# Kernel optimization log

Measured on AMD Instinct MI355X. Metric: run time of the kernel, lower is better.

Reference implementation:

```python
import jax, jax.numpy as jnp
import numpy as np

L, T, D = 3, 65536, 256


def setup_inputs() -> dict:
    key = jax.random.key(0)
    ks = jax.random.split(key, 10)
    stdv = 1.0 / np.sqrt(D)
    u = lambda k, shape: jax.random.uniform(k, shape, jnp.float32, -stdv, stdv)
    return {
        "story": jax.random.normal(ks[0], (T, D), jnp.float32),
        "question": jax.random.normal(ks[1], (D,), jnp.float32),
        "Wz_f": u(ks[2], (L, D, D)),
        "bz_f": u(ks[3], (L, D)),
        "Wh_f": u(ks[4], (L, 2 * D, D)),
        "bh_f": u(ks[5], (L, D)),
        "Wz_b": u(ks[6], (L, D, D)),
        "bz_b": u(ks[7], (L, D)),
        "Wh_b": u(ks[8], (L, 2 * D, D)),
        "bh_b": u(ks[9], (L, D)),
    }


def _qrn_dir(x, q, Wz, bz, Wh, bh):
    """One QRN layer in one direction. x, q: [T, D]. Returns h states [T, D]."""
    z = jax.nn.sigmoid((x * q) @ Wz + bz)                      # [T, D]
    h_tilde = jnp.tanh(jnp.concatenate([x, q], axis=-1) @ Wh + bh)  # [T, D]
    a = 1.0 - z            # multiplicative factor on h_prev
    b = z * h_tilde        # additive term
    # linear recurrence h_t = a_t * h_{t-1} + b_t, h_0 = 0 -> associative scan
    def comb(c1, c2):
        a1, b1 = c1
        a2, b2 = c2
        return a1 * a2, a2 * b1 + b2
    _, h = jax.lax.associative_scan(comb, (a, b), axis=0)
    return h  # h[t] = hidden state after statement t


def reference(story, question, Wz_f, bz_f, Wh_f, bh_f, Wz_b, bz_b, Wh_b, bh_b):
    q = jnp.broadcast_to(question, story.shape)  # layer-0 question per step
    for layer in range(L):
        h_fwd = _qrn_dir(story, q, Wz_f[layer], bz_f[layer], Wh_f[layer], bh_f[layer])
        # backward direction: reversed story with correspondingly reversed questions
        h_bwd_rev = _qrn_dir(story[::-1], q[::-1], Wz_b[layer], bz_b[layer],
                             Wh_b[layer], bh_b[layer])
        if layer < L - 1:
            # q_{t}^{k+1} = h_fwd_t + h_bwd_t (aligned back to forward order)
            q = h_fwd + h_bwd_rev[::-1]
    return h_fwd[-1]  # final forward hidden state of last layer, [D]
```

## Files before the change

### kernel.cpp

```cpp
#include <hip/hip_runtime.h>
#include <hip/hip_bf16.h>
#include <math.h>

#define D    256
#define BT   128
#define GN   128
#define NSEG 32

typedef unsigned short u16;
typedef unsigned int   u32;
typedef __attribute__((ext_vector_type(8))) short short8;
typedef __attribute__((ext_vector_type(4))) float floatx4;

__device__ __forceinline__ float b2f(u16 v) {
    union { unsigned u; float f; } x; x.u = ((unsigned)v) << 16; return x.f;
}
__device__ __forceinline__ u16 f2b(float f) {
    union { unsigned u; float f; } x; x.f = f;
    unsigned lsb = (x.u >> 16) & 1;
    x.u += 0x7fffu + lsb;
    return (u16)(x.u >> 16);
}
__device__ __forceinline__ float sigm(float x) {
    return __builtin_amdgcn_rcpf(1.0f + __expf(-x));
}
__device__ __forceinline__ float tanhfast(float x) {
    return 1.0f - 2.0f * __builtin_amdgcn_rcpf(__expf(2.0f * x) + 1.0f);
}
__device__ __forceinline__ void async16(const u16* g, u16* l) {
    __builtin_amdgcn_global_load_lds(
        (const __attribute__((address_space(1))) unsigned int*)g,
        (__attribute__((address_space(3))) unsigned int*)l, 16, 0, 0);
}

__global__ __launch_bounds__(256) void wtrans_kernel(
    const float* __restrict__ question,
    const float* __restrict__ Wz_f, const float* __restrict__ Wh_f,
    const float* __restrict__ Wz_b, const float* __restrict__ Wh_b,
    u16* __restrict__ wt)
{
    int id = blockIdx.x * 256 + threadIdx.x;
    int combo = id / (3 * 65536);
    int rem   = id % (3 * 65536);
    int m = rem >> 16;
    int e = rem & 65535;
    int k = e >> 8, n = e & 255;
    int l   = combo < 3 ? combo : combo - 3;
    int dir = combo < 3 ? 0 : 1;
    float v;
    if (m == 0) {
        const float* Wz = dir ? Wz_b : Wz_f;
        v = Wz[((size_t)l * D + k) * D + n];
        if (l == 0) v *= question[k];
    } else {
        const float* Wh = dir ? Wh_b : Wh_f;
        int kk = (m == 2) ? (k + D) : k;
        v = Wh[((size_t)l * 2 * D + kk) * D + n];
    }
    wt[(size_t)combo * 3 * 65536 + (size_t)m * 65536 + (size_t)n * D + k] = f2b(v);
}

__global__ __launch_bounds__(256) void bias0_kernel(
    const float* __restrict__ question,
    const float* __restrict__ Wh_f, const float* __restrict__ Wh_b,
    const float* __restrict__ bh_f, const float* __restrict__ bh_b,
    float* __restrict__ bh0f, float* __restrict__ bh0b)
{
    const float* Wh = blockIdx.x ? Wh_b : Wh_f;
    const float* bh = blockIdx.x ? bh_b : bh_f;
    float* out = blockIdx.x ? bh0b : bh0f;
    int n = threadIdx.x;
    float acc = bh[n];
    for (int k = 0; k < D; ++k)
        acc = fmaf(question[k], Wh[(size_t)(D + k) * D + n], acc);
    out[n] = acc;
}

__global__ __launch_bounds__(256) void prep0_kernel(
    const float* __restrict__ story, u16* __restrict__ xb)
{
    long id = (long)blockIdx.x * 256 + threadIdx.x;
    const float* xp = story + id * 8;
    float4 xa = *(const float4*)xp;
    float4 xc = *(const float4*)(xp + 4);
    float xv[8] = {xa.x, xa.y, xa.z, xa.w, xc.x, xc.y, xc.z, xc.w};
    short8 xs;
    #pragma unroll
    for (int i = 0; i < 8; ++i) xs[i] = (short)f2b(xv[i]);
    *(short8*)(xb + id * 8) = xs;
}

struct StageS {
    u16 ax [2][BT * 32]; u16 aq [2][BT * 32]; u16 axq[2][BT * 32];
    u16 bz_[GN * 32]; u16 bx_[GN * 32]; u16 bq_[GN * 32];
};
struct Stage0 {
    u16 ax [2][BT * 32];
    u16 bz_[GN * 32]; u16 bx_[GN * 32];
};
struct EpiP  { float segA[NSEG][GN]; float segB[NSEG][GN]; };
union __align__(16) SharedP  { StageS st; EpiP ep; };
union __align__(16) SharedP0 { Stage0 st; EpiP ep; };

__device__ __forceinline__ void gate_epilogue(
    EpiP& ep, int tid, int t0, int n0,
    floatx4 (&accz)[4][2], floatx4 (&acch)[4][2],
    const float* bz, const float* bh,
    float* aggA, float* aggB, u32* abg, int FWD)
{
    const int lane = tid & 63, w = tid >> 6;
    const int wr = w & 1, wc = w >> 1;
    const int lr = lane & 15, quad = lane >> 4;

    float bzn[2], bhn[2];
    #pragma unroll
    for (int ct = 0; ct < 2; ++ct) {
        int n = n0 + wc * 32 + ct * 16 + lr;
        bzn[ct] = bz[n]; bhn[ct] = bh[n];
    }
    float av[4][2][4], bvv[4][2][4];
    #pragma unroll
    for (int rt = 0; rt < 4; ++rt) {
        #pragma unroll
        for (int ct = 0; ct < 2; ++ct) {
            #pragma unroll
            for (int r = 0; r < 4; ++r) {
                float z  = sigm(accz[rt][ct][r] + bzn[ct]);
                float ht = tanhfast(acch[rt][ct][r] + bhn[ct]);
                av[rt][ct][r]  = 1.0f - z;
                bvv[rt][ct][r] = z * ht;
            }
            float A = 1.f, B = 0.f;
            if (FWD) {
                #pragma unroll
                for (int r = 0; r < 4; ++r) { A = av[rt][ct][r] * A; B = fmaf(av[rt][ct][r], B, bvv[rt][ct][r]); }
            } else {
                #pragma unroll
                for (int r = 3; r >= 0; --r) { A = av[rt][ct][r] * A; B = fmaf(av[rt][ct][r], B, bvv[rt][ct][r]); }
            }
            int seg = wr * 16 + rt * 4 + quad;
            int col = wc * 32 + ct * 16 + lr;
            ep.segA[seg][col] = A;
            ep.segB[seg][col] = B;
        }
    }
    __syncthreads();

    if (tid < GN) {
        float A = 1.f, B = 0.f;
        if (FWD) {
            #pragma unroll
            for (int sg = 0; sg < NSEG; ++sg) {
                float a = ep.segA[sg][tid], b = ep.segB[sg][tid];
                ep.segA[sg][tid] = A; ep.segB[sg][tid] = B;
                A = a * A; B = fmaf(a, B, b);
            }
        } else {
            #pragma unroll
            for (int sg = NSEG - 1; sg >= 0; --sg) {
                float a = ep.segA[sg][tid], b = ep.segB[sg][tid];
                ep.segA[sg][tid] = A; ep.segB[sg][tid] = B;
                A = a * A; B = fmaf(a, B, b);
            }
        }
        int c = t0 / BT;
        aggA[(size_t)c * D + n0 + tid] = A;
        aggB[(size_t)c * D + n0 + tid] = B;
    }

    if (abg) {
        __syncthreads();
        #pragma unroll
        for (int rt = 0; rt < 4; ++rt) {
            #pragma unroll
            for (int ct = 0; ct < 2; ++ct) {
                int seg = wr * 16 + rt * 4 + quad;
                int col = wc * 32 + ct * 16 + lr;
                float Pa = ep.segA[seg][col];
                float Pb = ep.segB[seg][col];
                size_t base = (size_t)(t0 + wr * 64 + rt * 16 + quad * 4) * D + n0 + col;
                if (FWD) {
                    #pragma unroll
                    for (int r = 0; r < 4; ++r) {
                        Pa = av[rt][ct][r] * Pa;
                        Pb = fmaf(av[rt][ct][r], Pb, bvv[rt][ct][r]);
                        abg[base + (size_t)r * D] = (u32)f2b(Pa) | ((u32)f2b(Pb) << 16);
                    }
                } else {
                    #pragma unroll
                    for (int r = 3; r >= 0; --r) {
                        Pa = av[rt][ct][r] * Pa;
                        Pb = fmaf(av[rt][ct][r], Pb, bvv[rt][ct][r]);
                        abg[base + (size_t)r * D] = (u32)f2b(Pa) | ((u32)f2b(Pb) << 16);
                    }
                }
            }
        }
    }
}

__device__ __forceinline__ void gemm_body(
    SharedP& sh, int tid, int c, int n0,
    const u16* xbg, const u16* qg, const u16* xqg, const u16* wt,
    const float* bz, const float* bh,
    float* aggA, float* aggB, u32* abg, int FWD)
{
    const int t0   = c * BT;
    const int lane = tid & 63, w = tid >> 6;
    const int wr = w & 1, wc = w >> 1;
    const int lr   = lane & 15, quad = lane >> 4;

    const int swA   = (quad ^ ((lr >> 1) & 3)) * 8;
    const int offA0 = (wr * 64 + lr) * 32 + swA;
    const int offB0 = (wc * 32 + lr) * 32 + swA;

    floatx4 accz[4][2], acch[4][2];
    #pragma unroll
    for (int rt = 0; rt < 4; ++rt)
        #pragma unroll
        for (int ct = 0; ct < 2; ++ct) {
            accz[rt][ct] = (floatx4){0.f,0.f,0.f,0.f};
            acch[rt][ct] = (floatx4){0.f,0.f,0.f,0.f};
        }

    const int lb = (tid & ~63) * 8;

    const int arow = tid >> 2;
    const int agg_ = (tid & 3) ^ ((arow >> 1) & 3);
    const size_t goA = (size_t)(t0 + arow) * D + agg_ * 8;
    const size_t goB = (size_t)(n0 + arow) * D + agg_ * 8;
    const u16* pax  = xbg + goA;
    const u16* paq  = qg  + goA;
    const u16* paxq = xqg + goA;
    const u16* pbz  = wt + goB;
    const u16* pbx  = wt + 65536  + goB;
    const u16* pbq  = wt + 131072 + goB;

    async16(pax , sh.st.ax [0] + lb);
    async16(paq , sh.st.aq [0] + lb);
    async16(paxq, sh.st.axq[0] + lb);

    #pragma unroll
    for (int kk = 0; kk < 8; ++kk) {
        const int cur = kk & 1, nxt = cur ^ 1;
        const int k0 = kk * 32;
        async16(pbz + k0, sh.st.bz_ + lb);
        async16(pbx + k0, sh.st.bx_ + lb);
        async16(pbq + k0, sh.st.bq_ + lb);
        if (kk < 7) {
            async16(pax  + k0 + 32, sh.st.ax [nxt] + lb);
            async16(paq  + k0 + 32, sh.st.aq [nxt] + lb);
            async16(paxq + k0 + 32, sh.st.axq[nxt] + lb);
            asm volatile("s_waitcnt vmcnt(3)" ::: "memory");
        } else {
            asm volatile("s_waitcnt vmcnt(0)" ::: "memory");
        }
        __builtin_amdgcn_s_barrier();
        asm volatile("" ::: "memory");

        short8 vz[2], vx[2], vq[2];
        #pragma unroll
        for (int ct = 0; ct < 2; ++ct) {
            vz[ct] = *(const short8*)(sh.st.bz_ + offB0 + ct * 512);
            vx[ct] = *(const short8*)(sh.st.bx_ + offB0 + ct * 512);
            vq[ct] = *(const short8*)(sh.st.bq_ + offB0 + ct * 512);
        }
        #pragma unroll
        for (int rt = 0; rt < 4; ++rt) {
            short8 fxq = *(const short8*)(sh.st.axq[cur] + offA0 + rt * 512);
            short8 fx  = *(const short8*)(sh.st.ax [cur] + offA0 + rt * 512);
            short8 fq  = *(const short8*)(sh.st.aq [cur] + offA0 + rt * 512);
            #pragma unroll
            for (int ct = 0; ct < 2; ++ct) {
                accz[rt][ct] = __builtin_amdgcn_mfma_f32_16x16x32_bf16(fxq, vz[ct], accz[rt][ct], 0, 0, 0);
                acch[rt][ct] = __builtin_amdgcn_mfma_f32_16x16x32_bf16(fx , vx[ct], acch[rt][ct], 0, 0, 0);
                acch[rt][ct] = __builtin_amdgcn_mfma_f32_16x16x32_bf16(fq , vq[ct], acch[rt][ct], 0, 0, 0);
            }
        }
        asm volatile("" ::: "memory");
        __builtin_amdgcn_s_barrier();
        asm volatile("" ::: "memory");
    }

    gate_epilogue(sh.ep, tid, t0, n0, accz, acch, bz, bh, aggA, aggB, abg, FWD);
}

__device__ __forceinline__ void gemm0_body(
    SharedP0& sh, int tid, int c, int n0,
    const u16* xbg, const u16* wt,
    const float* bz, const float* bh0,
    float* aggA, float* aggB, u32* abg, int FWD)
{
    const int t0   = c * BT;
    const int lane = tid & 63, w = tid >> 6;
    const int wr = w & 1, wc = w >> 1;
    const int lr   = lane & 15, quad = lane >> 4;

    const int swA   = (quad ^ ((lr >> 1) & 3)) * 8;
    const int offA0 = (wr * 64 + lr) * 32 + swA;
    const int offB0 = (wc * 32 + lr) * 32 + swA;

    floatx4 accz[4][2], acch[4][2];
    #pragma unroll
    for (int rt = 0; rt < 4; ++rt)
        #pragma unroll
        for (int ct = 0; ct < 2; ++ct) {
            accz[rt][ct] = (floatx4){0.f,0.f,0.f,0.f};
            acch[rt][ct] = (floatx4){0.f,0.f,0.f,0.f};
        }

    const int lb = (tid & ~63) * 8;
    const int arow = tid >> 2;
    const int agg_ = (tid & 3) ^ ((arow >> 1) & 3);
    const size_t goA = (size_t)(t0 + arow) * D + agg_ * 8;
    const size_t goB = (size_t)(n0 + arow) * D + agg_ * 8;
    const u16* pax = xbg + goA;
    const u16* pbz = wt + goB;
    const u16* pbx = wt + 65536 + goB;

    async16(pax, sh.st.ax[0] + lb);

    #pragma unroll
    for (int kk = 0; kk < 8; ++kk) {
        const int cur = kk & 1, nxt = cur ^ 1;
        const int k0 = kk * 32;
        async16(pbz + k0, sh.st.bz_ + lb);
        async16(pbx + k0, sh.st.bx_ + lb);
        if (kk < 7) {
            async16(pax + k0 + 32, sh.st.ax[nxt] + lb);
            asm volatile("s_waitcnt vmcnt(1)" ::: "memory");
        } else {
            asm volatile("s_waitcnt vmcnt(0)" ::: "memory");
        }
        __builtin_amdgcn_s_barrier();
        asm volatile("" ::: "memory");

        short8 vz[2], vx[2];
        #pragma unroll
        for (int ct = 0; ct < 2; ++ct) {
            vz[ct] = *(const short8*)(sh.st.bz_ + offB0 + ct * 512);
            vx[ct] = *(const short8*)(sh.st.bx_ + offB0 + ct * 512);
        }
        #pragma unroll
        for (int rt = 0; rt < 4; ++rt) {
            short8 fx = *(const short8*)(sh.st.ax[cur] + offA0 + rt * 512);
            #pragma unroll
            for (int ct = 0; ct < 2; ++ct) {
                accz[rt][ct] = __builtin_amdgcn_mfma_f32_16x16x32_bf16(fx, vz[ct], accz[rt][ct], 0, 0, 0);
                acch[rt][ct] = __builtin_amdgcn_mfma_f32_16x16x32_bf16(fx, vx[ct], acch[rt][ct], 0, 0, 0);
            }
        }
        asm volatile("" ::: "memory");
        __builtin_amdgcn_s_barrier();
        asm volatile("" ::: "memory");
    }

    gate_epilogue(sh.ep, tid, t0, n0, accz, acch, bz, bh0, aggA, aggB, abg, FWD);
}

template<int FWD, int ABOUT>
__global__ __launch_bounds__(512, 4) void qrn_g5(
    const u16* __restrict__ xbg, const u16* __restrict__ qg,
    const u16* __restrict__ xqg, const u16* __restrict__ wt,
    const float* __restrict__ bz, const float* __restrict__ bh,
    float* __restrict__ aggA, float* __restrict__ aggB,
    u32* __restrict__ abg)
{
    __shared__ SharedP sh;
    const int tid  = threadIdx.x;
    const int bid  = (int)blockIdx.x;
    const int gidx = (bid & 7) * 128 + (bid >> 3);
    gemm_body(sh, tid, gidx >> 1, (gidx & 1) * GN,
              xbg, qg, xqg, wt, bz, bh, aggA, aggB, ABOUT ? abg : nullptr, FWD);
}

__global__ __launch_bounds__(512, 4) void qrn_gboth(
    const u16* __restrict__ xbg, const u16* __restrict__ qg,
    const u16* __restrict__ xqg,
    const u16* __restrict__ wtF, const u16* __restrict__ wtB,
    const float* __restrict__ bzf, const float* __restrict__ bhf,
    const float* __restrict__ bzb, const float* __restrict__ bhb,
    float* __restrict__ aggAf, float* __restrict__ aggBf,
    float* __restrict__ aggAb, float* __restrict__ aggBb,
    u32* __restrict__ abf, u32* __restrict__ abb)
{
    __shared__ SharedP sh;
    const int tid  = threadIdx.x;
    const int half = (int)blockIdx.x >> 10;
    const int bid  = (int)blockIdx.x & 1023;
    const int gidx = (bid & 7) * 128 + (bid >> 3);
    gemm_body(sh, tid, gidx >> 1, (gidx & 1) * GN,
              xbg, qg, xqg,
              half ? wtB : wtF,
              half ? bzb : bzf, half ? bhb : bhf,
              half ? aggAb : aggAf, half ? aggBb : aggBf,
              half ? abb : abf, half ? 0 : 1);
}

template<int FWD>
__global__ __launch_bounds__(512, 4) void qrn_g0(
    const u16* __restrict__ xbg, const u16* __restrict__ wt,
    const float* __restrict__ bz, const float* __restrict__ bh0,
    float* __restrict__ aggA, float* __restrict__ aggB,
    u32* __restrict__ abg)
{
    __shared__ SharedP0 sh;
    const int tid  = threadIdx.x;
    const int bid  = (int)blockIdx.x;
    const int gidx = (bid & 7) * 128 + (bid >> 3);
    gemm0_body(sh, tid, gidx >> 1, (gidx & 1) * GN,
               xbg, wt, bz, bh0, aggA, aggB, abg, FWD);
}

__global__ __launch_bounds__(512, 4) void qrn_g0both(
    const u16* __restrict__ xbg,
    const u16* __restrict__ wtF, const u16* __restrict__ wtB,
    const float* __restrict__ bzf, const float* __restrict__ bh0f,
    const float* __restrict__ bzb, const float* __restrict__ bh0b,
    float* __restrict__ aggAf, float* __restrict__ aggBf,
    float* __restrict__ aggAb, float* __restrict__ aggBb,
    u32* __restrict__ abf, u32* __restrict__ abb)
{
    __shared__ SharedP0 sh;
    const int tid  = threadIdx.x;
    const int half = (int)blockIdx.x >> 10;
    const int bid  = (int)blockIdx.x & 1023;
    const int gidx = (bid & 7) * 128 + (bid >> 3);
    gemm0_body(sh, tid, gidx >> 1, (gidx & 1) * GN,
               xbg,
               half ? wtB : wtF,
               half ? bzb : bzf, half ? bh0b : bh0f,
               half ? aggAb : aggAf, half ? aggBb : aggBf,
               half ? abb : abf, half ? 0 : 1);
}

__global__ __launch_bounds__(256) void replay2_fb(
    const u32* __restrict__ abf, const u32* __restrict__ abb,
    const float* __restrict__ hinif, const float* __restrict__ hinib,
    const u16* __restrict__ xb, u16* __restrict__ qout, u16* __restrict__ xq,
    int total8)
{
    for (int id = (int)blockIdx.x * 256 + (int)threadIdx.x; id < total8;
         id += (int)gridDim.x * 256) {
        int t  = id >> 5;
        int n0 = (id & 31) * 8;
        int c  = t >> 7;
        size_t o  = (size_t)t * D + n0;
        size_t hc = (size_t)c * D + n0;
        uint4 f0 = *(const uint4*)(abf + o);
        uint4 f1 = *(const uint4*)(abf + o + 4);
        uint4 g0 = *(const uint4*)(abb + o);
        uint4 g1 = *(const uint4*)(abb + o + 4);
        float4 hf0 = *(const float4*)(hinif + hc);
        float4 hf1 = *(const float4*)(hinif + hc + 4);
        float4 hb0 = *(const float4*)(hinib + hc);
        float4 hb1 = *(const float4*)(hinib + hc + 4);
        short8 xv = *(const short8*)(xb + o);
        u32 fa[8] = {f0.x, f0.y, f0.z, f0.w, f1.x, f1.y, f1.z, f1.w};
        u32 ga[8] = {g0.x, g0.y, g0.z, g0.w, g1.x, g1.y, g1.z, g1.w};
        float hfv[8] = {hf0.x, hf0.y, hf0.z, hf0.w, hf1.x, hf1.y, hf1.z, hf1.w};
        float hbv[8] = {hb0.x, hb0.y, hb0.z, hb0.w, hb1.x, hb1.y, hb1.z, hb1.w};
        short8 qs, xqs;
        #pragma unroll
        for (int i = 0; i < 8; ++i) {
            float hF = fmaf(b2f((u16)(fa[i] & 0xffff)), hfv[i], b2f((u16)(fa[i] >> 16)));
            float hB = fmaf(b2f((u16)(ga[i] & 0xffff)), hbv[i], b2f((u16)(ga[i] >> 16)));
            u16 qb = f2b(hF + hB);
            qs[i]  = (short)qb;
            xqs[i] = (short)f2b(b2f((u16)xv[i]) * b2f(qb));
        }
        *(short8*)(qout + o) = qs;
        *(short8*)(xq + o)   = xqs;
    }
}

__global__ __launch_bounds__(256) void replay2_f(
    const u32* __restrict__ abg, const float* __restrict__ hini,
    u16* __restrict__ qout, int total8)
{
    for (int id = (int)blockIdx.x * 256 + (int)threadIdx.x; id < total8;
         id += (int)gridDim.x * 256) {
        int t  = id >> 5;
        int n0 = (id & 31) * 8;
        int c  = t >> 7;
        size_t o  = (size_t)t * D + n0;
        size_t hc = (size_t)c * D + n0;
        uint4 f0 = *(const uint4*)(abg + o);
        uint4 f1 = *(const uint4*)(abg + o + 4);
        float4 hf0 = *(const float4*)(hini + hc);
        float4 hf1 = *(const float4*)(hini + hc + 4);
        u32 fa[8] = {f0.x, f0.y, f0.z, f0.w, f1.x, f1.y, f1.z, f1.w};
        float hfv[8] = {hf0.x, hf0.y, hf0.z, hf0.w, hf1.x, hf1.y, hf1.z, hf1.w};
        short8 qs;
        #pragma unroll
        for (int i = 0; i < 8; ++i) {
            float hF = fmaf(b2f((u16)(fa[i] & 0xffff)), hfv[i], b2f((u16)(fa[i] >> 16)));
            qs[i] = (short)f2b(hF);
        }
        *(short8*)(qout + o) = qs;
    }
}

__global__ __launch_bounds__(256) void replay2_b(
    const u32* __restrict__ abg, const float* __restrict__ hini,
    const u16* __restrict__ xb, u16* __restrict__ qout, u16* __restrict__ xq,
    int total8)
{
    for (int id = (int)blockIdx.x * 256 + (int)threadIdx.x; id < total8;
         id += (int)gridDim.x * 256) {
        int t  = id >> 5;
        int n0 = (id & 31) * 8;
        int c  = t >> 7;
        size_t o  = (size_t)t * D + n0;
        size_t hc = (size_t)c * D + n0;
        uint4 g0 = *(const uint4*)(abg + o);
        uint4 g1 = *(const uint4*)(abg + o + 4);
        float4 hb0 = *(const float4*)(hini + hc);
        float4 hb1 = *(const float4*)(hini + hc + 4);
        short8 qold = *(const short8*)(qout + o);
        short8 xv   = *(const short8*)(xb + o);
        u32 ga[8] = {g0.x, g0.y, g0.z, g0.w, g1.x, g1.y, g1.z, g1.w};
        float hbv[8] = {hb0.x, hb0.y, hb0.z, hb0.w, hb1.x, hb1.y, hb1.z, hb1.w};
        short8 qs, xqs;
        #pragma unroll
        for (int i = 0; i < 8; ++i) {
            float hB = fmaf(b2f((u16)(ga[i] & 0xffff)), hbv[i], b2f((u16)(ga[i] >> 16)));
            float qn = b2f((u16)qold[i]) + hB;
            u16 qb = f2b(qn);
            qs[i]  = (short)qb;
            xqs[i] = (short)f2b(b2f((u16)xv[i]) * b2f(qb));
        }
        *(short8*)(qout + o) = qs;
        *(short8*)(xq + o)   = xqs;
    }
}

__device__ __forceinline__ void scan_body(
    const float* aggA, const float* aggB, float* hinit, float* out_final,
    int fwd, int nch, int n, int tid)
{
    __shared__ float sA[256], sB[256];
    const int per = nch >> 8;
    float lA[4], lB[4];
    float A = 1.f, B = 0.f;
    for (int j = 0; j < per; ++j) {
        int pidx = tid * per + j;
        int c = fwd ? pidx : (nch - 1 - pidx);
        float a = aggA[(size_t)c * D + n];
        float b = aggB[(size_t)c * D + n];
        lA[j] = a; lB[j] = b;
        A = a * A;
        B = fmaf(a, B, b);
    }
    sA[tid] = A; sB[tid] = B;
    __syncthreads();
    for (int off = 1; off < 256; off <<= 1) {
        float pA = 1.f, pB = 0.f;
        if (tid >= off) { pA = sA[tid - off]; pB = sB[tid - off]; }
        __syncthreads();
        if (tid >= off) {
            float cA = sA[tid], cB = sB[tid];
            sA[tid] = pA * cA;
            sB[tid] = fmaf(cA, pB, cB);
        }
        __syncthreads();
    }
    float eB = (tid > 0) ? sB[tid - 1] : 0.f;
    for (int j = 0; j < per; ++j) {
        int pidx = tid * per + j;
        int c = fwd ? pidx : (nch - 1 - pidx);
        hinit[(size_t)c * D + n] = eB;
        eB = fmaf(lA[j], eB, lB[j]);
    }
    if (out_final != nullptr && tid == 0) out_final[n] = sB[255];
}

__global__ __launch_bounds__(256) void scan_p2_kernel(
    const float* __restrict__ aggA, const float* __restrict__ aggB,
    float* __restrict__ hinit, float* __restrict__ out_final, int fwd, int nch)
{
    scan_body(aggA, aggB, hinit, out_final, fwd, nch, blockIdx.x, threadIdx.x);
}

__global__ __launch_bounds__(256) void scan_dual_kernel(
    const float* __restrict__ aggAf, const float* __restrict__ aggBf, float* __restrict__ hf,
    const float* __restrict__ aggAb, const float* __restrict__ aggBb, float* __restrict__ hb,
    int nch)
{
    int b = blockIdx.x;
    int fwd = (b < D) ? 1 : 0;
    int n = fwd ? b : (b - D);
    scan_body(fwd ? aggAf : aggAb, fwd ? aggBf : aggBb,
              fwd ? hf : hb, nullptr, fwd, nch, n, threadIdx.x);
}

extern "C" void kernel_launch(void* const* d_in, const int* in_sizes, int n_in,
                              void* d_out, int out_size, void* d_ws, size_t ws_size,
                              hipStream_t stream) {
    const float* story    = (const float*)d_in[0];
    const float* question = (const float*)d_in[1];
    const float* Wz_f = (const float*)d_in[2];
    const float* bz_f = (const float*)d_in[3];
    const float* Wh_f = (const float*)d_in[4];
    const float* bh_f = (const float*)d_in[5];
    const float* Wz_b = (const float*)d_in[6];
    const float* bz_b = (const float*)d_in[7];
    const float* Wh_b = (const float*)d_in[8];
    const float* bh_b = (const float*)d_in[9];

    const int T    = in_sizes[0] / D;
    const int NCH  = T / BT;
    const size_t TD = (size_t)T * D;
    const size_t WTE = 5 * 3 * 65536;
    const int total8 = T * 32;

    const size_t needF = 3 * TD * 2 + WTE * 2 + 2 * TD * 4
                       + (size_t)4 * NCH * D * 4 + 2 * D * 4 + 4096;
    const bool planF = ws_size >= needF;

    dim3 blk(256);
    dim3 gblk(512);
    dim3 gGrid((unsigned)(NCH * 2));
    dim3 g2Grid((unsigned)(NCH * 4));
    dim3 rGrid(2048);
    dim3 pGrid((unsigned)(TD / 8 / 256));

    if (planF) {
        u16* xb = (u16*)d_ws;
        u16* q  = xb + TD;
        u16* xq = q  + TD;
        u16* wt = xq + TD;
        u32* abf = (u32*)(wt + WTE);
        u32* abb = abf + TD;
        float* aggAf = (float*)(abb + TD);
        float* aggBf = aggAf + (size_t)NCH * D;
        float* aggAb = aggBf + (size_t)NCH * D;
        float* aggBb = aggAb + (size_t)NCH * D;
        float* bh0f  = aggBb + (size_t)NCH * D;
        float* bh0b  = bh0f + D;
        float* hinif = aggBf;
        float* hinib = aggBb;

        wtrans_kernel<<<dim3(5 * 3 * 65536 / 256), blk, 0, stream>>>(
            question, Wz_f, Wh_f, Wz_b, Wh_b, wt);
        bias0_kernel<<<dim3(2), blk, 0, stream>>>(
            question, Wh_f, Wh_b, bh_f, bh_b, bh0f, bh0b);
        prep0_kernel<<<pGrid, blk, 0, stream>>>(story, xb);

        for (int l = 0; l < 3; ++l) {
            const u16*   wtf = wt + (size_t)l * 3 * 65536;
            const float* bzf = bz_f + (size_t)l * D;
            const float* bhf = bh_f + (size_t)l * D;

            if (l == 2) {
                qrn_g5<1,0><<<gGrid, gblk, 0, stream>>>(
                    xb, q, xq, wtf, bzf, bhf, aggAf, aggBf, nullptr);
                scan_p2_kernel<<<dim3(D), blk, 0, stream>>>(
                    aggAf, aggBf, hinif, (float*)d_out, 1, NCH);
                break;
            }
            const u16*   wtb = wt + (size_t)(3 + l) * 3 * 65536;
            const float* bzb = bz_b + (size_t)l * D;
            const float* bhb = bh_b + (size_t)l * D;

            if (l == 0) {
                qrn_g0both<<<g2Grid, gblk, 0, stream>>>(
                    xb, wtf, wtb, bzf, bh0f, bzb, bh0b,
                    aggAf, aggBf, aggAb, aggBb, abf, abb);
            } else {
                qrn_gboth<<<g2Grid, gblk, 0, stream>>>(
                    xb, q, xq, wtf, wtb, bzf, bhf, bzb, bhb,
                    aggAf, aggBf, aggAb, aggBb, abf, abb);
            }
            scan_dual_kernel<<<dim3(2 * D), blk, 0, stream>>>(
                aggAf, aggBf, hinif, aggAb, aggBb, hinib, NCH);
            replay2_fb<<<rGrid, blk, 0, stream>>>(
                abf, abb, hinif, hinib, xb, q, xq, total8);
        }
    } else {
        u16* xb = (u16*)d_ws;
        u16* qA = xb + TD;
        u16* qB = qA + TD;
        u16* xq = qB + TD;
        u16* wt = xq + TD;
        u32*   ab   = (u32*)(wt + WTE);
        float* aggA = (float*)(ab + TD);
        float* aggB = aggA + (size_t)NCH * D;
        float* bh0f = aggB + (size_t)NCH * D;
        float* bh0b = bh0f + D;
        float* hini = aggB;

        wtrans_kernel<<<dim3(5 * 3 * 65536 / 256), blk, 0, stream>>>(
            question, Wz_f, Wh_f, Wz_b, Wh_b, wt);
        bias0_kernel<<<dim3(2), blk, 0, stream>>>(
            question, Wh_f, Wh_b, bh_f, bh_b, bh0f, bh0b);
        prep0_kernel<<<pGrid, blk, 0, stream>>>(story, xb);

        const u16* qcur  = qA;
        u16*       qnext = qB;

        for (int l = 0; l < 3; ++l) {
            const u16*   wtf = wt + (size_t)l * 3 * 65536;
            const float* bzf = bz_f + (size_t)l * D;
            const float* bhf = bh_f + (size_t)l * D;

            if (l == 2) {
                qrn_g5<1,0><<<gGrid, gblk, 0, stream>>>(
                    xb, qcur, xq, wtf, bzf, bhf, aggA, aggB, nullptr);
                scan_p2_kernel<<<dim3(D), blk, 0, stream>>>(
                    aggA, aggB, hini, (float*)d_out, 1, NCH);
                break;
            }
            const u16*   wtb = wt + (size_t)(3 + l) * 3 * 65536;
            const float* bzb = bz_b + (size_t)l * D;
            const float* bhb = bh_b + (size_t)l * D;

            if (l == 0) {
                qrn_g0<1><<<gGrid, gblk, 0, stream>>>(
                    xb, wtf, bzf, bh0f, aggA, aggB, ab);
                scan_p2_kernel<<<dim3(D), blk, 0, stream>>>(aggA, aggB, hini, nullptr, 1, NCH);
                replay2_f<<<rGrid, blk, 0, stream>>>(ab, hini, qnext, total8);

                qrn_g0<0><<<gGrid, gblk, 0, stream>>>(
                    xb, wtb, bzb, bh0b, aggA, aggB, ab);
                scan_p2_kernel<<<dim3(D), blk, 0, stream>>>(aggA, aggB, hini, nullptr, 0, NCH);
                replay2_b<<<rGrid, blk, 0, stream>>>(ab, hini, xb, qnext, xq, total8);
            } else {
                qrn_g5<1,1><<<gGrid, gblk, 0, stream>>>(
                    xb, qcur, xq, wtf, bzf, bhf, aggA, aggB, ab);
                scan_p2_kernel<<<dim3(D), blk, 0, stream>>>(aggA, aggB, hini, nullptr, 1, NCH);
                replay2_f<<<rGrid, blk, 0, stream>>>(ab, hini, qnext, total8);

                qrn_g5<0,1><<<gGrid, gblk, 0, stream>>>(
                    xb, qcur, xq, wtb, bzb, bhb, aggA, aggB, ab);
                scan_p2_kernel<<<dim3(D), blk, 0, stream>>>(aggA, aggB, hini, nullptr, 0, NCH);
                replay2_b<<<rGrid, blk, 0, stream>>>(ab, hini, xb, qnext, xq, total8);
            }
            const u16* ts = qcur; qcur = qnext; qnext = (u16*)ts;
        }
    }
}
```

Baseline: 413.9 us.

## Compute x*q in GEMM registers and double-buffer weight tiles

Drops the materialised x*q bf16 tensor. The gate GEMM now forms x*q from the x and q fragments already staged in LDS, and the replay kernels no longer read x or write xq. This removes one T×D bf16 read and write per layer-direction. Separately, the weight B-tiles are now double-buffered so they prefetch one k-step ahead along with the A tiles. The costs are extra VALU work per fragment (convert, multiply, round) inside the MFMA loop and more LDS for the doubled weight buffers.

```diff
diff --git a/kernel.cpp b/kernel.cpp
--- a/kernel.cpp
+++ b/kernel.cpp
@@ -31,6 +31,13 @@
     __builtin_amdgcn_global_load_lds(
         (const __attribute__((address_space(1))) unsigned int*)g,
         (__attribute__((address_space(3))) unsigned int*)l, 16, 0, 0);
+}
+__device__ __forceinline__ short8 bmul8(short8 a, short8 b) {
+    short8 r;
+    #pragma unroll
+    for (int i = 0; i < 8; ++i)
+        r[i] = (short)f2b(b2f((u16)a[i]) * b2f((u16)b[i]));
+    return r;
 }
 
 __global__ __launch_bounds__(256) void wtrans_kernel(
@@ -91,12 +98,12 @@
 }
 
 struct StageS {
-    u16 ax [2][BT * 32]; u16 aq [2][BT * 32]; u16 axq[2][BT * 32];
-    u16 bz_[GN * 32]; u16 bx_[GN * 32]; u16 bq_[GN * 32];
+    u16 ax [2][BT * 32]; u16 aq [2][BT * 32];
+    u16 bz_[2][GN * 32]; u16 bx_[2][GN * 32]; u16 bq_[2][GN * 32];
 };
 struct Stage0 {
     u16 ax [2][BT * 32];
-    u16 bz_[GN * 32]; u16 bx_[GN * 32];
+    u16 bz_[2][GN * 32]; u16 bx_[2][GN * 32];
 };
 struct EpiP  { float segA[NSEG][GN]; float segB[NSEG][GN]; };
 union __align__(16) SharedP  { StageS st; EpiP ep; };
@@ -201,7 +208,7 @@
 
 __device__ __forceinline__ void gemm_body(
     SharedP& sh, int tid, int c, int n0,
-    const u16* xbg, const u16* qg, const u16* xqg, const u16* wt,
+    const u16* xbg, const u16* qg, const u16* wt,
     const float* bz, const float* bh,
     float* aggA, float* aggB, u32* abg, int FWD)
 {
@@ -231,27 +238,26 @@
     const size_t goB = (size_t)(n0 + arow) * D + agg_ * 8;
     const u16* pax  = xbg + goA;
     const u16* paq  = qg  + goA;
-    const u16* paxq = xqg + goA;
     const u16* pbz  = wt + goB;
     const u16* pbx  = wt + 65536  + goB;
     const u16* pbq  = wt + 131072 + goB;
 
-    async16(pax , sh.st.ax [0] + lb);
-    async16(paq , sh.st.aq [0] + lb);
-    async16(paxq, sh.st.axq[0] + lb);
+    auto stage = [&](int buf, int k0) {
+        async16(pax + k0, sh.st.ax [buf] + lb);
+        async16(paq + k0, sh.st.aq [buf] + lb);
+        async16(pbz + k0, sh.st.bz_[buf] + lb);
+        async16(pbx + k0, sh.st.bx_[buf] + lb);
+        async16(pbq + k0, sh.st.bq_[buf] + lb);
+    };
+
+    stage(0, 0);
 
     #pragma unroll
     for (int kk = 0; kk < 8; ++kk) {
-        const int cur = kk & 1, nxt = cur ^ 1;
-        const int k0 = kk * 32;
-        async16(pbz + k0, sh.st.bz_ + lb);
-        async16(pbx + k0, sh.st.bx_ + lb);
-        async16(pbq + k0, sh.st.bq_ + lb);
+        const int cur = kk & 1;
         if (kk < 7) {
-            async16(pax  + k0 + 32, sh.st.ax [nxt] + lb);
-            async16(paq  + k0 + 32, sh.st.aq [nxt] + lb);
-            async16(paxq + k0 + 32, sh.st.axq[nxt] + lb);
-            asm volatile("s_waitcnt vmcnt(3)" ::: "memory");
+            stage(cur ^ 1, (kk + 1) * 32);
+            asm volatile("s_waitcnt vmcnt(5)" ::: "memory");
         } else {
             asm volatile("s_waitcnt vmcnt(0)" ::: "memory");
         }
@@ -261,15 +267,15 @@
         short8 vz[2], vx[2], vq[2];
         #pragma unroll
         for (int ct = 0; ct < 2; ++ct) {
-            vz[ct] = *(const short8*)(sh.st.bz_ + offB0 + ct * 512);
-            vx[ct] = *(const short8*)(sh.st.bx_ + offB0 + ct * 512);
-            vq[ct] = *(const short8*)(sh.st.bq_ + offB0 + ct * 512);
+            vz[ct] = *(const short8*)(sh.st.bz_[cur] + offB0 + ct * 512);
+            vx[ct] = *(const short8*)(sh.st.bx_[cur] + offB0 + ct * 512);
+            vq[ct] = *(const short8*)(sh.st.bq_[cur] + offB0 + ct * 512);
         }
         #pragma unroll
         for (int rt = 0; rt < 4; ++rt) {
-            short8 fxq = *(const short8*)(sh.st.axq[cur] + offA0 + rt * 512);
-            short8 fx  = *(const short8*)(sh.st.ax [cur] + offA0 + rt * 512);
-            short8 fq  = *(const short8*)(sh.st.aq [cur] + offA0 + rt * 512);
+            short8 fx  = *(const short8*)(sh.st.ax[cur] + offA0 + rt * 512);
+            short8 fq  = *(const short8*)(sh.st.aq[cur] + offA0 + rt * 512);
+            short8 fxq = bmul8(fx, fq);
             #pragma unroll
             for (int ct = 0; ct < 2; ++ct) {
                 accz[rt][ct] = __builtin_amdgcn_mfma_f32_16x16x32_bf16(fxq, vz[ct], accz[rt][ct], 0, 0, 0);
@@ -318,17 +324,20 @@
     const u16* pbz = wt + goB;
     const u16* pbx = wt + 65536 + goB;
 
-    async16(pax, sh.st.ax[0] + lb);
+    auto stage = [&](int buf, int k0) {
+        async16(pax + k0, sh.st.ax [buf] + lb);
+        async16(pbz + k0, sh.st.bz_[buf] + lb);
+        async16(pbx + k0, sh.st.bx_[buf] + lb);
+    };
+
+    stage(0, 0);
 
     #pragma unroll
     for (int kk = 0; kk < 8; ++kk) {
-        const int cur = kk & 1, nxt = cur ^ 1;
-        const int k0 = kk * 32;
-        async16(pbz + k0, sh.st.bz_ + lb);
-        async16(pbx + k0, sh.st.bx_ + lb);
+        const int cur = kk & 1;
         if (kk < 7) {
-            async16(pax + k0 + 32, sh.st.ax[nxt] + lb);
-            asm volatile("s_waitcnt vmcnt(1)" ::: "memory");
+            stage(cur ^ 1, (kk + 1) * 32);
+            asm volatile("s_waitcnt vmcnt(3)" ::: "memory");
         } else {
             asm volatile("s_waitcnt vmcnt(0)" ::: "memory");
         }
@@ -338,8 +347,8 @@
         short8 vz[2], vx[2];
         #pragma unroll
         for (int ct = 0; ct < 2; ++ct) {
-            vz[ct] = *(const short8*)(sh.st.bz_ + offB0 + ct * 512);
-            vx[ct] = *(const short8*)(sh.st.bx_ + offB0 + ct * 512);
+            vz[ct] = *(const short8*)(sh.st.bz_[cur] + offB0 + ct * 512);
+            vx[ct] = *(const short8*)(sh.st.bx_[cur] + offB0 + ct * 512);
         }
         #pragma unroll
         for (int rt = 0; rt < 4; ++rt) {
@@ -361,7 +370,7 @@
 template<int FWD, int ABOUT>
 __global__ __launch_bounds__(512, 4) void qrn_g5(
     const u16* __restrict__ xbg, const u16* __restrict__ qg,
-    const u16* __restrict__ xqg, const u16* __restrict__ wt,
+    const u16* __restrict__ wt,
     const float* __restrict__ bz, const float* __restrict__ bh,
     float* __restrict__ aggA, float* __restrict__ aggB,
     u32* __restrict__ abg)
@@ -371,12 +380,11 @@
     const int bid  = (int)blockIdx.x;
     const int gidx = (bid & 7) * 128 + (bid >> 3);
     gemm_body(sh, tid, gidx >> 1, (gidx & 1) * GN,
-              xbg, qg, xqg, wt, bz, bh, aggA, aggB, ABOUT ? abg : nullptr, FWD);
+              xbg, qg, wt, bz, bh, aggA, aggB, ABOUT ? abg : nullptr, FWD);
 }
 
 __global__ __launch_bounds__(512, 4) void qrn_gboth(
     const u16* __restrict__ xbg, const u16* __restrict__ qg,
-    const u16* __restrict__ xqg,
     const u16* __restrict__ wtF, const u16* __restrict__ wtB,
     const float* __restrict__ bzf, const float* __restrict__ bhf,
     const float* __restrict__ bzb, const float* __restrict__ bhb,
@@ -390,7 +398,7 @@
     const int bid  = (int)blockIdx.x & 1023;
     const int gidx = (bid & 7) * 128 + (bid >> 3);
     gemm_body(sh, tid, gidx >> 1, (gidx & 1) * GN,
-              xbg, qg, xqg,
+              xbg, qg,
               half ? wtB : wtF,
               half ? bzb : bzf, half ? bhb : bhf,
               half ? aggAb : aggAf, half ? aggBb : aggBf,
@@ -437,8 +445,7 @@
 __global__ __launch_bounds__(256) void replay2_fb(
     const u32* __restrict__ abf, const u32* __restrict__ abb,
     const float* __restrict__ hinif, const float* __restrict__ hinib,
-    const u16* __restrict__ xb, u16* __restrict__ qout, u16* __restrict__ xq,
-    int total8)
+    u16* __restrict__ qout, int total8)
 {
     for (int id = (int)blockIdx.x * 256 + (int)threadIdx.x; id < total8;
          id += (int)gridDim.x * 256) {
@@ -455,22 +462,18 @@
         float4 hf1 = *(const float4*)(hinif + hc + 4);
         float4 hb0 = *(const float4*)(hinib + hc);
         float4 hb1 = *(const float4*)(hinib + hc + 4);
-        short8 xv = *(const short8*)(xb + o);
         u32 fa[8] = {f0.x, f0.y, f0.z, f0.w, f1.x, f1.y, f1.z, f1.w};
         u32 ga[8] = {g0.x, g0.y, g0.z, g0.w, g1.x, g1.y, g1.z, g1.w};
         float hfv[8] = {hf0.x, hf0.y, hf0.z, hf0.w, hf1.x, hf1.y, hf1.z, hf1.w};
         float hbv[8] = {hb0.x, hb0.y, hb0.z, hb0.w, hb1.x, hb1.y, hb1.z, hb1.w};
-        short8 qs, xqs;
+        short8 qs;
         #pragma unroll
         for (int i = 0; i < 8; ++i) {
             float hF = fmaf(b2f((u16)(fa[i] & 0xffff)), hfv[i], b2f((u16)(fa[i] >> 16)));
             float hB = fmaf(b2f((u16)(ga[i] & 0xffff)), hbv[i], b2f((u16)(ga[i] >> 16)));
-            u16 qb = f2b(hF + hB);
-            qs[i]  = (short)qb;
-            xqs[i] = (short)f2b(b2f((u16)xv[i]) * b2f(qb));
+            qs[i] = (short)f2b(hF + hB);
         }
         *(short8*)(qout + o) = qs;
-        *(short8*)(xq + o)   = xqs;
     }
 }
 
@@ -503,8 +506,7 @@
 
 __global__ __launch_bounds__(256) void replay2_b(
     const u32* __restrict__ abg, const float* __restrict__ hini,
-    const u16* __restrict__ xb, u16* __restrict__ qout, u16* __restrict__ xq,
-    int total8)
+    u16* __restrict__ qout, int total8)
 {
     for (int id = (int)blockIdx.x * 256 + (int)threadIdx.x; id < total8;
          id += (int)gridDim.x * 256) {
@@ -518,20 +520,15 @@
         float4 hb0 = *(const float4*)(hini + hc);
         float4 hb1 = *(const float4*)(hini + hc + 4);
         short8 qold = *(const short8*)(qout + o);
-        short8 xv   = *(const short8*)(xb + o);
         u32 ga[8] = {g0.x, g0.y, g0.z, g0.w, g1.x, g1.y, g1.z, g1.w};
         float hbv[8] = {hb0.x, hb0.y, hb0.z, hb0.w, hb1.x, hb1.y, hb1.z, hb1.w};
-        short8 qs, xqs;
+        short8 qs;
         #pragma unroll
         for (int i = 0; i < 8; ++i) {
             float hB = fmaf(b2f((u16)(ga[i] & 0xffff)), hbv[i], b2f((u16)(ga[i] >> 16)));
-            float qn = b2f((u16)qold[i]) + hB;
-            u16 qb = f2b(qn);
-            qs[i]  = (short)qb;
-            xqs[i] = (short)f2b(b2f((u16)xv[i]) * b2f(qb));
+            qs[i] = (short)f2b(b2f((u16)qold[i]) + hB);
         }
         *(short8*)(qout + o) = qs;
-        *(short8*)(xq + o)   = xqs;
     }
 }
 
@@ -614,7 +611,7 @@
     const size_t WTE = 5 * 3 * 65536;
     const int total8 = T * 32;
 
-    const size_t needF = 3 * TD * 2 + WTE * 2 + 2 * TD * 4
+    const size_t needF = 2 * TD * 2 + WTE * 2 + 2 * TD * 4
                        + (size_t)4 * NCH * D * 4 + 2 * D * 4 + 4096;
     const bool planF = ws_size >= needF;
 
@@ -628,8 +625,7 @@
     if (planF) {
         u16* xb = (u16*)d_ws;
         u16* q  = xb + TD;
-        u16* xq = q  + TD;
-        u16* wt = xq + TD;
+        u16* wt = q  + TD;
         u32* abf = (u32*)(wt + WTE);
         u32* abb = abf + TD;
         float* aggAf = (float*)(abb + TD);
@@ -654,7 +650,7 @@
 
             if (l == 2) {
                 qrn_g5<1,0><<<gGrid, gblk, 0, stream>>>(
-                    xb, q, xq, wtf, bzf, bhf, aggAf, aggBf, nullptr);
+                    xb, q, wtf, bzf, bhf, aggAf, aggBf, nullptr);
                 scan_p2_kernel<<<dim3(D), blk, 0, stream>>>(
                     aggAf, aggBf, hinif, (float*)d_out, 1, NCH);
                 break;
@@ -669,20 +665,19 @@
                     aggAf, aggBf, aggAb, aggBb, abf, abb);
             } else {
                 qrn_gboth<<<g2Grid, gblk, 0, stream>>>(
-                    xb, q, xq, wtf, wtb, bzf, bhf, bzb, bhb,
+                    xb, q, wtf, wtb, bzf, bhf, bzb, bhb,
                     aggAf, aggBf, aggAb, aggBb, abf, abb);
             }
             scan_dual_kernel<<<dim3(2 * D), blk, 0, stream>>>(
                 aggAf, aggBf, hinif, aggAb, aggBb, hinib, NCH);
             replay2_fb<<<rGrid, blk, 0, stream>>>(
-                abf, abb, hinif, hinib, xb, q, xq, total8);
+                abf, abb, hinif, hinib, q, total8);
         }
     } else {
         u16* xb = (u16*)d_ws;
         u16* qA = xb + TD;
         u16* qB = qA + TD;
-        u16* xq = qB + TD;
-        u16* wt = xq + TD;
+        u16* wt = qB + TD;
         u32*   ab   = (u32*)(wt + WTE);
         float* aggA = (float*)(ab + TD);
         float* aggB = aggA + (size_t)NCH * D;
@@ -706,7 +701,7 @@
 
             if (l == 2) {
                 qrn_g5<1,0><<<gGrid, gblk, 0, stream>>>(
-                    xb, qcur, xq, wtf, bzf, bhf, aggA, aggB, nullptr);
+                    xb, qcur, wtf, bzf, bhf, aggA, aggB, nullptr);
                 scan_p2_kernel<<<dim3(D), blk, 0, stream>>>(
                     aggA, aggB, hini, (float*)d_out, 1, NCH);
                 break;
@@ -724,17 +719,17 @@
                 qrn_g0<0><<<gGrid, gblk, 0, stream>>>(
                     xb, wtb, bzb, bh0b, aggA, aggB, ab);
                 scan_p2_kernel<<<dim3(D), blk, 0, stream>>>(aggA, aggB, hini, nullptr, 0, NCH);
-                replay2_b<<<rGrid, blk, 0, stream>>>(ab, hini, xb, qnext, xq, total8);
+                replay2_b<<<rGrid, blk, 0, stream>>>(ab, hini, qnext, total8);
             } else {
                 qrn_g5<1,1><<<gGrid, gblk, 0, stream>>>(
-                    xb, qcur, xq, wtf, bzf, bhf, aggA, aggB, ab);
+                    xb, qcur, wtf, bzf, bhf, aggA, aggB, ab);
                 scan_p2_kernel<<<dim3(D), blk, 0, stream>>>(aggA, aggB, hini, nullptr, 1, NCH);
                 replay2_f<<<rGrid, blk, 0, stream>>>(ab, hini, qnext, total8);
 
                 qrn_g5<0,1><<<gGrid, gblk, 0, stream>>>(
-                    xb, qcur, xq, wtb, bzb, bhb, aggA, aggB, ab);
+                    xb, qcur, wtb, bzb, bhb, aggA, aggB, ab);
                 scan_p2_kernel<<<dim3(D), blk, 0, stream>>>(aggA, aggB, hini, nullptr, 0, NCH);
-                replay2_b<<<rGrid, blk, 0, stream>>>(ab, hini, xb, qnext, xq, total8);
+                replay2_b<<<rGrid, blk, 0, stream>>>(ab, hini, qnext, total8);
             }
             const u16* ts = qcur; qcur = qnext; qnext = (u16*)ts;
         }
```

After: 443.5 us. +7.2%, slower.
